# Kernel tuning notes

Hardware: AMD Instinct MI355X
Metric: run time of the kernel (lower is better)

Reference implementation:

```python
import jax, jax.numpy as jnp
import numpy as np

I, H, T, B, T2 = 512, 1024, 384, 128, 384  # input_size, hidden, cell seq, batch, gru seq


def _gru_layer(x, h0, Wih, Whh, bih, bhh):
    """PyTorch-style GRU layer. x: (B,T,Cin), h0: (B,H). Returns (out (B,T,H), h_last (B,H))."""
    xg = jnp.einsum('btc,gc->btg', x, Wih) + bih  # (B,T,3H) input projections, precomputed

    def step(h, xg_t):
        gh = h @ Whh.T + bhh                      # (B,3H)
        xr, xz, xn = jnp.split(xg_t, 3, axis=-1)
        hr, hz, hn = jnp.split(gh, 3, axis=-1)
        r = jax.nn.sigmoid(xr + hr)
        z = jax.nn.sigmoid(xz + hz)
        n = jnp.tanh(xn + r * hn)
        h_new = (1.0 - z) * n + z * h
        return h_new, h_new

    h_last, ys = jax.lax.scan(step, h0, jnp.swapaxes(xg, 0, 1))  # scan over T
    return jnp.swapaxes(ys, 0, 1), h_last


def setup_inputs() -> dict:
    key = jax.random.key(0)
    ks = jax.random.split(key, 16)
    bound = 1.0 / np.sqrt(H)
    u = lambda kk, shape: jax.random.uniform(kk, shape, jnp.float32, -bound, bound)
    return {
        'input_seq': jax.random.normal(ks[0], (T, B, I), jnp.float32),
        'rand_input': jax.random.normal(ks[1], (B, T2, H), jnp.float32),
        'h0': jax.random.normal(ks[2], (2, B, H), jnp.float32),
        'cell_Wih': u(ks[3], (3 * H, I)),
        'cell_Whh': u(ks[4], (3 * H, H)),
        'cell_bih': u(ks[5], (3 * H,)),
        'cell_bhh': u(ks[6], (3 * H,)),
        'gru_Wih0': u(ks[7], (3 * H, H)),
        'gru_Whh0': u(ks[8], (3 * H, H)),
        'gru_bih0': u(ks[9], (3 * H,)),
        'gru_bhh0': u(ks[10], (3 * H,)),
        'gru_Wih1': u(ks[11], (3 * H, H)),
        'gru_Whh1': u(ks[12], (3 * H, H)),
        'gru_bih1': u(ks[13], (3 * H,)),
        'gru_bhh1': u(ks[14], (3 * H,)),
        'lin_W': u(ks[15], (1, H)),
        'lin_b': jnp.zeros((1,), jnp.float32),
    }


def reference(input_seq, rand_input, h0,
              cell_Wih, cell_Whh, cell_bih, cell_bhh,
              gru_Wih0, gru_Whh0, gru_bih0, gru_bhh0,
              gru_Wih1, gru_Whh1, gru_bih1, gru_bhh1,
              lin_W, lin_b):
    # --- GRUCellModel: cell called with hx=None each step -> hidden is zeros every
    # step, so the whole 'recurrence' vectorizes over T (h @ Whh == 0).
    xg = jnp.einsum('tbi,gi->tbg', input_seq, cell_Wih) + cell_bih  # (T,B,3H)
    xr, xz, xn = jnp.split(xg, 3, axis=-1)
    br, bz, bn = jnp.split(cell_bhh, 3)
    r = jax.nn.sigmoid(xr + br)
    z = jax.nn.sigmoid(xz + bz)
    n = jnp.tanh(xn + r * bn)
    gru_cell_output = jnp.swapaxes((1.0 - z) * n, 0, 1)  # (B,T,H); unused downstream (as in source)

    # --- GRUModel: ignores its input, runs 2-layer GRU on internal random tensors.
    out0, _ = _gru_layer(rand_input, h0[0], gru_Wih0, gru_Whh0, gru_bih0, gru_bhh0)
    gru_output, _ = _gru_layer(out0, h0[1], gru_Wih1, gru_Whh1, gru_bih1, gru_bhh1)

    s = gru_output.shape[1] // 3
    outputs = jnp.concatenate([gru_output[:, 0:s], gru_output[:, s:2 * s], gru_output[:, 2 * s:]], axis=1)

    # second GRU run, zero initial hidden; keep last layer's final hidden
    zero_h = jnp.zeros((outputs.shape[0], H), outputs.dtype)
    o0, _ = _gru_layer(outputs, zero_h, gru_Wih0, gru_Whh0, gru_bih0, gru_bhh0)
    _, h_last = _gru_layer(o0, zero_h, gru_Wih1, gru_Whh1, gru_bih1, gru_bhh1)

    predictions = h_last @ lin_W.T + lin_b  # (B,1)
    # anchor: keep the (dead-code) GRUCell branch alive under jit without changing values
    predictions = predictions + 0.0 * jnp.sum(gru_cell_output)
    return predictions
```

## Files before the change

kernel.cpp:

```cpp
#include <hip/hip_runtime.h>
#include <math.h>

typedef __attribute__((ext_vector_type(8))) __bf16          bf16x8;
typedef __attribute__((ext_vector_type(8))) unsigned short  ushort8;
typedef __attribute__((ext_vector_type(4))) float           f32x4;
typedef __attribute__((ext_vector_type(4))) unsigned int    u32x4;

constexpr int Bb = 128, Hh = 1024, Tt = 384, BH = Bb * Hh;
constexpr int NWG = 256, BLK = 256;

constexpr size_t SLOT_B  = 524288;
constexpr size_t OFF_H   = 1024;
constexpr size_t OFF_W   = OFF_H + 8 * SLOT_B;
constexpr size_t WBLK_B  = 12288;
constexpr size_t OFF_X   = OFF_W + 4096ull * WBLK_B;
constexpr size_t WS_FULL = OFF_X + 384ull * SLOT_B;

__device__ __forceinline__ float b2f(unsigned short h) {
    unsigned u = ((unsigned)h) << 16;
    return __builtin_bit_cast(float, u);
}
__device__ __forceinline__ void split_bf16(float x, unsigned short& hi, unsigned short& lo) {
    unsigned u  = __builtin_bit_cast(unsigned, x);
    unsigned uh = u & 0xFFFF0000u;
    hi = (unsigned short)(uh >> 16);
    float rem = x - __builtin_bit_cast(float, uh);
    unsigned ur = __builtin_bit_cast(unsigned, rem);
    ur += 0x7FFFu + ((ur >> 16) & 1u);
    lo = (unsigned short)(ur >> 16);
}
__device__ __forceinline__ void split8(const float* src, ushort8& h8, ushort8& l8) {
    const float4* p4 = (const float4*)src;
    float4 a = p4[0], b = p4[1];
    float v[8] = {a.x, a.y, a.z, a.w, b.x, b.y, b.z, b.w};
    #pragma unroll
    for (int m = 0; m < 8; ++m) { unsigned short h, l; split_bf16(v[m], h, l); h8[m] = h; l8[m] = l; }
}
__device__ __forceinline__ void async16(const void* g, void* l) {
    __builtin_amdgcn_global_load_lds(
        (const __attribute__((address_space(1))) unsigned int*)g,
        (__attribute__((address_space(3))) unsigned int*)l, 16, 0, 0);
}


__global__ void wsplit_kernel(const float* __restrict__ W0i, const float* __restrict__ W0h,
                              const float* __restrict__ W1i, const float* __restrict__ W1h,
                              char* __restrict__ wbuf) {
    int t = blockIdx.x * 256 + threadIdx.x;
    if (t >= 4 * 64 * 16 * 48 * 8) return;
    int g8 = t & 7;
    int r  = (t >> 3) % 48;
    int rest = (t >> 3) / 48;
    int kcg = rest & 15, jwg = (rest >> 4) & 63, m = rest >> 10;
    const float* W = (m == 0) ? W0i : (m == 1) ? W0h : (m == 2) ? W1i : W1h;
    int ct = r >> 4, jl = r & 15;
    const float* src = W + (size_t)((ct << 10) + jwg * 16 + jl) * 1024 + kcg * 64 + g8 * 8;
    ushort8 h8, l8; split8(src, h8, l8);
    int ks = (g8 >> 2) & 1, kg = g8 & 3, lane = kg * 16 + jl;
    char* blk = wbuf + (size_t)rest * WBLK_B;
    int off0 = (ct * 4 + ks) * 1024 + lane * 16;
    *(ushort8*)(blk + off0)        = h8;
    *(ushort8*)(blk + off0 + 2048) = l8;
}

__global__ void xsplit_kernel(const float* __restrict__ xin, char* __restrict__ xb) {
    int t = blockIdx.x * 256 + threadIdx.x;
    if (t >= 384 * 128 * 128) return;
    int g8 = t & 127, b = (t >> 7) & 127, tau = t >> 14;
    const float* src = xin + ((size_t)b * 384 + tau) * 1024 + g8 * 8;
    ushort8 h8, l8; split8(src, h8, l8);
    int kcg = g8 >> 3, gin = g8 & 7;
    int ks = (gin >> 2) & 1, kg = gin & 3;
    int lane = kg * 16 + (b & 15);
    int BI0 = kcg * 32 + (b >> 5) * 8 + ((b >> 4) & 1) * 4 + ks;
    char* dst = xb + (size_t)tau * SLOT_B + (size_t)BI0 * 1024 + lane * 16;
    *(ushort8*)dst          = h8;
    *(ushort8*)(dst + 2048) = l8;
}

__global__ void hinit_kernel(const float* __restrict__ h0, char* __restrict__ ws) {
    int t = blockIdx.x * 256 + threadIdx.x;
    if (t == 0) *(unsigned*)ws = 0;
    if (t >= 4 * 128 * 128) return;
    char* hs = ws + OFF_H;
    int g8 = t & 127, b = (t >> 7) & 127, si = t >> 14;
    ushort8 h8, l8;
    if (si < 2) {
        split8(h0 + (size_t)si * BH + (size_t)b * 1024 + g8 * 8, h8, l8);
    } else {
        #pragma unroll
        for (int m = 0; m < 8; ++m) { h8[m] = 0; l8[m] = 0; }
    }
    int kcg = g8 >> 3, gin = g8 & 7;
    int ks = (gin >> 2) & 1, kg = gin & 3;
    int lane = kg * 16 + (b & 15);
    int BI0 = kcg * 32 + (b >> 5) * 8 + ((b >> 4) & 1) * 4 + ks;
    char* dst = hs + (size_t)(si * 2 + 1) * SLOT_B + (size_t)BI0 * 1024 + lane * 16;
    *(ushort8*)dst          = h8;
    *(ushort8*)(dst + 2048) = l8;
}


__device__ __forceinline__ void grid_barrier(unsigned* cnt, unsigned target) {
    __syncthreads();
    if (threadIdx.x == 0) {
        __hip_atomic_fetch_add(cnt, 1u, __ATOMIC_RELEASE, __HIP_MEMORY_SCOPE_AGENT);
        while (__hip_atomic_load(cnt, __ATOMIC_RELAXED, __HIP_MEMORY_SCOPE_AGENT) < target)
            __builtin_amdgcn_s_sleep(1);
    }
    __syncthreads();
}

#define WAITVM(N) asm volatile("s_waitcnt vmcnt(" #N ")" ::: "memory")

#define GITER(CH, SLOT, ACC, WN, DOISS)                                  \
    WAITVM(WN);                                                          \
    asm volatile("" ::: "memory");                                       \
    __builtin_amdgcn_s_barrier();                                        \
    __builtin_amdgcn_sched_barrier(0);                                   \
    if (DOISS) { issueA((CH) + 3, ar[((SLOT) + 3) & 3]);                 \
                 issueB((CH) + 3, ((SLOT) + 3) & 3); }                   \
    computeC(ar[SLOT], (SLOT), ACC);

template<bool XS>
__global__ __launch_bounds__(BLK, 2) void gru_persistent(
    const float* __restrict__ xin,
    const float* __restrict__ bih0, const float* __restrict__ bhh0,
    const float* __restrict__ bih1, const float* __restrict__ bhh1,
    unsigned* __restrict__ cnt, char* __restrict__ ws)
{
    __shared__ char Bs[4][12288];

    char*       hs = ws + OFF_H;
    const char* wb = ws + OFF_W;
    const char* xs = ws + OFF_X;

    const int bid = blockIdx.x, layer = bid >> 6, jwg = bid & 63, jbase = jwg * 16;
    const int tid = threadIdx.x, lane = tid & 63, rg = tid >> 6;

    const float* bih = (layer & 1) ? bih1 : bih0;
    const float* bhh = (layer & 1) ? bhh1 : bhh0;
    const int jl = lane & 15;
    const int jcol = jbase + jl;
    const float b_ir = bih[jcol],          b_hr = bhh[jcol];
    const float b_iz = bih[Hh + jcol],     b_hz = bhh[Hh + jcol];
    const float b_in = bih[2 * Hh + jcol], b_hn = bhh[2 * Hh + jcol];

    const int kcg_j = jcol >> 6, ks_j = (jcol >> 5) & 1, kg_j = (jcol >> 3) & 3, e_j = jcol & 7;
    const int baseBI = kcg_j * 32 + rg * 8 + ks_j;
    auto hoff = [&](int rb, int pl, int q) -> size_t {
        return (size_t)(baseBI + rb * 4 + pl * 2) * 1024
             + (size_t)(kg_j * 16 + (lane >> 4) * 4 + q) * 16 + e_j * 2;
    };

    float hreg[8];
    const bool fb0 = (!XS) && (layer == 0);

    unsigned target = NWG;
    for (int s = 0; s < Tt + 3; ++s, target += NWG) {
        const int tau = s - layer;
        if (tau >= 0 && tau < Tt) {
            const char* Axb = (layer == 0) ? (xs + (size_t)tau * SLOT_B)
                                           : (hs + (size_t)(((layer - 1) * 2) + (tau & 1)) * SLOT_B);
            const char* Ahb = hs + (size_t)((layer * 2) + ((tau - 1) & 1)) * SLOT_B;
            char*       Hd  = hs + (size_t)((layer * 2) + (tau & 1)) * SLOT_B;

            if (tau == 0) {
                if (layer < 2) {
                    #pragma unroll
                    for (int rb = 0; rb < 2; ++rb)
                        #pragma unroll
                        for (int q = 0; q < 4; ++q) {
                            unsigned short hi = __hip_atomic_load(
                                (const unsigned short*)(Ahb + hoff(rb, 0, q)),
                                __ATOMIC_RELAXED, __HIP_MEMORY_SCOPE_AGENT);
                            unsigned short lo = __hip_atomic_load(
                                (const unsigned short*)(Ahb + hoff(rb, 1, q)),
                                __ATOMIC_RELAXED, __HIP_MEMORY_SCOPE_AGENT);
                            hreg[rb * 4 + q] = b2f(hi) + b2f(lo);
                        }
                    asm volatile("s_waitcnt vmcnt(0)" ::: "memory");
                } else {
                    #pragma unroll
                    for (int i = 0; i < 8; ++i) hreg[i] = 0.f;
                }
            }

            auto issueA = [&](int ch, u32x4* fr) {
                const char* base = ((ch < 16) ? Axb : Ahb)
                                 + ((size_t)(ch & 15) << 15) + (rg << 13) + (lane << 4);
                #pragma unroll
                for (int rb = 0; rb < 2; ++rb) {
                    const char* p = base + (rb << 12);
                    asm volatile("global_load_dwordx4 %0, %1, off sc0 sc1"             : "=v"(fr[rb*4+0]) : "v"(p));
                    asm volatile("global_load_dwordx4 %0, %1, off offset:1024 sc0 sc1" : "=v"(fr[rb*4+1]) : "v"(p));
                    asm volatile("global_load_dwordx4 %0, %1, off offset:2048 sc0 sc1" : "=v"(fr[rb*4+2]) : "v"(p));
                    asm volatile("global_load_dwordx4 %0, %1, off offset:3072 sc0 sc1" : "=v"(fr[rb*4+3]) : "v"(p));
                }
            };
            auto issueB = [&](int ch, int buf) {
                const int m = (layer & 1) * 2 + (ch < 16 ? 0 : 1);
                const char* Wb = wb + (size_t)(((m * 64 + jwg) << 4) + (ch & 15)) * WBLK_B;
                char* L = &Bs[buf][0];
                #pragma unroll
                for (int i = 0; i < 3; ++i) {
                    int seg = rg + i * 4;
                    async16(Wb + seg * 1024 + lane * 16, L + seg * 1024);
                }
            };
            auto fragX = [&](int ch, u32x4* fr) {
                const int kcg = ch & 15;
                #pragma unroll
                for (int rb = 0; rb < 2; ++rb)
                    #pragma unroll
                    for (int ks = 0; ks < 2; ++ks) {
                        int row = rg * 32 + rb * 16 + (lane & 15);
                        int k0  = kcg * 64 + ks * 32 + (lane >> 4) * 8;
                        ushort8 h8, l8;
                        split8(xin + ((size_t)row * 384 + tau) * 1024 + k0, h8, l8);
                        fr[rb * 4 + ks]     = __builtin_bit_cast(u32x4, h8);
                        fr[rb * 4 + 2 + ks] = __builtin_bit_cast(u32x4, l8);
                    }
            };
            auto computeC = [&](u32x4* fr, int buf, f32x4 (&acc)[2][3]) {
                const char* B = &Bs[buf][0];
                __builtin_amdgcn_s_setprio(1);
                #pragma unroll
                for (int ks = 0; ks < 2; ++ks) {
                    bf16x8 Bh[3], Bl[3];
                    #pragma unroll
                    for (int ct = 0; ct < 3; ++ct) {
                        Bh[ct] = __builtin_bit_cast(bf16x8, *(const ushort8*)(B + (ct*4 + ks)*1024 + lane*16));
                        Bl[ct] = __builtin_bit_cast(bf16x8, *(const ushort8*)(B + (ct*4 + 2 + ks)*1024 + lane*16));
                    }
                    #pragma unroll
                    for (int rb = 0; rb < 2; ++rb) {
                        bf16x8 Ah = __builtin_bit_cast(bf16x8, fr[rb*4 + ks]);
                        bf16x8 Al = __builtin_bit_cast(bf16x8, fr[rb*4 + 2 + ks]);
                        #pragma unroll
                        for (int ct = 0; ct < 3; ++ct) {
                            f32x4 c = acc[rb][ct];
                            c = __builtin_amdgcn_mfma_f32_16x16x32_bf16(Ah, Bh[ct], c, 0, 0, 0);
                            c = __builtin_amdgcn_mfma_f32_16x16x32_bf16(Al, Bh[ct], c, 0, 0, 0);
                            c = __builtin_amdgcn_mfma_f32_16x16x32_bf16(Ah, Bl[ct], c, 0, 0, 0);
                            acc[rb][ct] = c;
                        }
                    }
                }
                __builtin_amdgcn_s_setprio(0);
            };

            f32x4 accX[2][3], accH[2][3];
            const f32x4 zv = {0.f, 0.f, 0.f, 0.f};
            #pragma unroll
            for (int rb = 0; rb < 2; ++rb)
                #pragma unroll
                for (int ct = 0; ct < 3; ++ct) { accX[rb][ct] = zv; accH[rb][ct] = zv; }

            u32x4 ar[4][8];

            if (!fb0) {
                issueA(0, ar[0]); issueB(0, 0);
                issueA(1, ar[1]); issueB(1, 1);
                issueA(2, ar[2]); issueB(2, 2);
                for (int c4 = 0; c4 < 16; c4 += 4) {
                    GITER(c4 + 0, 0, accX, 22, true);
                    GITER(c4 + 1, 1, accX, 22, true);
                    GITER(c4 + 2, 2, accX, 22, true);
                    GITER(c4 + 3, 3, accX, 22, true);
                }
                for (int c4 = 16; c4 < 28; c4 += 4) {
                    GITER(c4 + 0, 0, accH, 22, true);
                    GITER(c4 + 1, 1, accH, 22, true);
                    GITER(c4 + 2, 2, accH, 22, true);
                    GITER(c4 + 3, 3, accH, 22, true);
                }
                GITER(28, 0, accH, 22, true);
                GITER(29, 1, accH, 22, false);
                GITER(30, 2, accH, 11, false);
                GITER(31, 3, accH, 0,  false);
            } else {
                for (int ch = 0; ch < 32; ++ch) {
                    if (ch < 16) fragX(ch, ar[0]); else issueA(ch, ar[0]);
                    issueB(ch, 0);
                    asm volatile("s_waitcnt vmcnt(0)" ::: "memory");
                    asm volatile("" ::: "memory");
                    __builtin_amdgcn_s_barrier();
                    __builtin_amdgcn_sched_barrier(0);
                    if (ch < 16) computeC(ar[0], 0, accX); else computeC(ar[0], 0, accH);
                    asm volatile("" ::: "memory");
                    __builtin_amdgcn_s_barrier();
                    asm volatile("" ::: "memory");
                }
            }

            #pragma unroll
            for (int rb = 0; rb < 2; ++rb)
                #pragma unroll
                for (int q = 0; q < 4; ++q) {
                    float rp = accX[rb][0][q] + accH[rb][0][q] + b_ir + b_hr;
                    float zp = accX[rb][1][q] + accH[rb][1][q] + b_iz + b_hz;
                    float xn = accX[rb][2][q] + b_in;
                    float hn = accH[rb][2][q] + b_hn;
                    float r  = 1.0f / (1.0f + expf(-rp));
                    float z  = 1.0f / (1.0f + expf(-zp));
                    float n  = tanhf(xn + r * hn);
                    float h  = (1.0f - z) * n + z * hreg[rb * 4 + q];
                    hreg[rb * 4 + q] = h;
                    unsigned short hi, lo; split_bf16(h, hi, lo);
                    __hip_atomic_store((unsigned short*)(Hd + hoff(rb, 0, q)), hi,
                                       __ATOMIC_RELAXED, __HIP_MEMORY_SCOPE_AGENT);
                    __hip_atomic_store((unsigned short*)(Hd + hoff(rb, 1, q)), lo,
                                       __ATOMIC_RELAXED, __HIP_MEMORY_SCOPE_AGENT);
                }
        }
        grid_barrier(cnt, target);
    }
}

__global__ void pred_kernel(const char* __restrict__ hs,
                            const float* __restrict__ linW,
                            const float* __restrict__ linb,
                            float* __restrict__ out) {
    const int b = blockIdx.x, l = threadIdx.x;
    const char* slot = hs + 7 * SLOT_B;
    const int rpart = (b >> 5) * 8 + ((b >> 4) & 1) * 4;
    float s = 0.f;
    for (int u = l; u < Hh; u += 64) {
        int BI0 = (u >> 6) * 32 + rpart + ((u >> 5) & 1);
        size_t o = (size_t)BI0 * 1024 + (size_t)(((u >> 3) & 3) * 16 + (b & 15)) * 16 + (u & 7) * 2;
        float hv = b2f(*(const unsigned short*)(slot + o))
                 + b2f(*(const unsigned short*)(slot + o + 2048));
        s += hv * linW[u];
    }
    #pragma unroll
    for (int off = 32; off > 0; off >>= 1) s += __shfl_down(s, off);
    if (l == 0) out[b] = s + linb[0];
}

extern "C" void kernel_launch(void* const* d_in, const int* in_sizes, int n_in,
                              void* d_out, int out_size, void* d_ws, size_t ws_size,
                              hipStream_t stream) {
    const float* rand_in = (const float*)d_in[1];
    const float* h0      = (const float*)d_in[2];
    const float* Wih0    = (const float*)d_in[7];
    const float* Whh0    = (const float*)d_in[8];
    const float* bih0    = (const float*)d_in[9];
    const float* bhh0    = (const float*)d_in[10];
    const float* Wih1    = (const float*)d_in[11];
    const float* Whh1    = (const float*)d_in[12];
    const float* bih1    = (const float*)d_in[13];
    const float* bhh1    = (const float*)d_in[14];
    const float* linW    = (const float*)d_in[15];
    const float* linb    = (const float*)d_in[16];
    float* out = (float*)d_out;

    char*     ws  = (char*)d_ws;
    unsigned* cnt = (unsigned*)d_ws;
    char*     hsl = ws + OFF_H;

    const bool xsl = (ws_size >= WS_FULL);

    wsplit_kernel<<<6144, 256, 0, stream>>>(Wih0, Whh0, Wih1, Whh1, ws + OFF_W);
    hinit_kernel<<<256, 256, 0, stream>>>(h0, ws);
    if (xsl) {
        xsplit_kernel<<<24576, 256, 0, stream>>>(rand_in, ws + OFF_X);
        gru_persistent<true><<<NWG, BLK, 0, stream>>>(rand_in, bih0, bhh0, bih1, bhh1, cnt, ws);
    } else {
        gru_persistent<false><<<NWG, BLK, 0, stream>>>(rand_in, bih0, bhh0, bih1, bhh1, cnt, ws);
    }
    pred_kernel<<<Bb, 64, 0, stream>>>(hsl, linW, linb, out);
}
```

Baseline: 14.61 ms.

## Retile GRU persistent kernel to 32 columns by 64 rows per workgroup

```diff
diff --git a/kernel.cpp b/kernel.cpp
--- a/kernel.cpp
+++ b/kernel.cpp
@@ -12,8 +12,8 @@
 constexpr size_t SLOT_B  = 524288;
 constexpr size_t OFF_H   = 1024;
 constexpr size_t OFF_W   = OFF_H + 8 * SLOT_B;
-constexpr size_t WBLK_B  = 12288;
-constexpr size_t OFF_X   = OFF_W + 4096ull * WBLK_B;
+constexpr size_t WBLK_B  = 24576;
+constexpr size_t OFF_X   = OFF_W + 2048ull * WBLK_B;
 constexpr size_t WS_FULL = OFF_X + 384ull * SLOT_B;
 
 __device__ __forceinline__ float b2f(unsigned short h) {
@@ -47,14 +47,15 @@
                               const float* __restrict__ W1i, const float* __restrict__ W1h,
                               char* __restrict__ wbuf) {
     int t = blockIdx.x * 256 + threadIdx.x;
-    if (t >= 4 * 64 * 16 * 48 * 8) return;
+    if (t >= 2048 * 96 * 8) return;
     int g8 = t & 7;
-    int r  = (t >> 3) % 48;
-    int rest = (t >> 3) / 48;
-    int kcg = rest & 15, jwg = (rest >> 4) & 63, m = rest >> 10;
+    int r  = (t >> 3) % 96;
+    int rest = (t >> 3) / 96;
+    int kcg = rest & 15, cg = (rest >> 4) & 31, m = rest >> 9;
     const float* W = (m == 0) ? W0i : (m == 1) ? W0h : (m == 2) ? W1i : W1h;
     int ct = r >> 4, jl = r & 15;
-    const float* src = W + (size_t)((ct << 10) + jwg * 16 + jl) * 1024 + kcg * 64 + g8 * 8;
+    int jh = ct / 3, g = ct % 3;
+    const float* src = W + (size_t)((g << 10) + cg * 32 + jh * 16 + jl) * 1024 + kcg * 64 + g8 * 8;
     ushort8 h8, l8; split8(src, h8, l8);
     int ks = (g8 >> 2) & 1, kg = g8 & 3, lane = kg * 16 + jl;
     char* blk = wbuf + (size_t)rest * WBLK_B;
@@ -123,34 +124,43 @@
     computeC(ar[SLOT], (SLOT), ACC);
 
 template<bool XS>
-__global__ __launch_bounds__(BLK, 2) void gru_persistent(
+__global__ __launch_bounds__(BLK, 1) void gru_persistent(
     const float* __restrict__ xin,
     const float* __restrict__ bih0, const float* __restrict__ bhh0,
     const float* __restrict__ bih1, const float* __restrict__ bhh1,
     unsigned* __restrict__ cnt, char* __restrict__ ws)
 {
-    __shared__ char Bs[4][12288];
+    __shared__ char Bs[4][24576];
 
     char*       hs = ws + OFF_H;
     const char* wb = ws + OFF_W;
     const char* xs = ws + OFF_X;
 
-    const int bid = blockIdx.x, layer = bid >> 6, jwg = bid & 63, jbase = jwg * 16;
-    const int tid = threadIdx.x, lane = tid & 63, rg = tid >> 6;
+    const int bid = blockIdx.x;
+    const int xcd = bid & 7, sl = bid >> 3;
+    const int pair = xcd * 16 + (sl >> 1), rq = sl & 1;
+    const int layer = pair >> 5, cg = pair & 31;
+    const int tid = threadIdx.x, lane = tid & 63, wv = tid >> 6;
 
     const float* bih = (layer & 1) ? bih1 : bih0;
     const float* bhh = (layer & 1) ? bhh1 : bhh0;
     const int jl = lane & 15;
-    const int jcol = jbase + jl;
-    const float b_ir = bih[jcol],          b_hr = bhh[jcol];
-    const float b_iz = bih[Hh + jcol],     b_hz = bhh[Hh + jcol];
-    const float b_in = bih[2 * Hh + jcol], b_hn = bhh[2 * Hh + jcol];
-
-    const int kcg_j = jcol >> 6, ks_j = (jcol >> 5) & 1, kg_j = (jcol >> 3) & 3, e_j = jcol & 7;
-    const int baseBI = kcg_j * 32 + rg * 8 + ks_j;
-    auto hoff = [&](int rb, int pl, int q) -> size_t {
-        return (size_t)(baseBI + rb * 4 + pl * 2) * 1024
-             + (size_t)(kg_j * 16 + (lane >> 4) * 4 + q) * 16 + e_j * 2;
+
+    int   kcg_j[2], ks_j[2], kg_j[2], e_j[2];
+    float b_ir[2], b_hr[2], b_iz[2], b_hz[2], b_in[2], b_hn[2];
+    #pragma unroll
+    for (int jh = 0; jh < 2; ++jh) {
+        int j = cg * 32 + jh * 16 + jl;
+        kcg_j[jh] = j >> 6; ks_j[jh] = (j >> 5) & 1; kg_j[jh] = (j >> 3) & 3; e_j[jh] = j & 7;
+        b_ir[jh] = bih[j];           b_hr[jh] = bhh[j];
+        b_iz[jh] = bih[Hh + j];      b_hz[jh] = bhh[Hh + j];
+        b_in[jh] = bih[2 * Hh + j];  b_hn[jh] = bhh[2 * Hh + j];
+    }
+    const int rowBI = (rq * 2 + (wv >> 1)) * 8 + (wv & 1) * 4;
+
+    auto hoff = [&](int jh, int pl, int q) -> size_t {
+        return (size_t)(kcg_j[jh] * 32 + rowBI + pl * 2 + ks_j[jh]) * 1024
+             + (size_t)(kg_j[jh] * 16 + (lane >> 4) * 4 + q) * 16 + e_j[jh] * 2;
     };
 
     float hreg[8];
@@ -168,16 +178,16 @@
             if (tau == 0) {
                 if (layer < 2) {
                     #pragma unroll
-                    for (int rb = 0; rb < 2; ++rb)
+                    for (int jh = 0; jh < 2; ++jh)
                         #pragma unroll
                         for (int q = 0; q < 4; ++q) {
                             unsigned short hi = __hip_atomic_load(
-                                (const unsigned short*)(Ahb + hoff(rb, 0, q)),
+                                (const unsigned short*)(Ahb + hoff(jh, 0, q)),
                                 __ATOMIC_RELAXED, __HIP_MEMORY_SCOPE_AGENT);
                             unsigned short lo = __hip_atomic_load(
-                                (const unsigned short*)(Ahb + hoff(rb, 1, q)),
+                                (const unsigned short*)(Ahb + hoff(jh, 1, q)),
                                 __ATOMIC_RELAXED, __HIP_MEMORY_SCOPE_AGENT);
-                            hreg[rb * 4 + q] = b2f(hi) + b2f(lo);
+                            hreg[jh * 4 + q] = b2f(hi) + b2f(lo);
                         }
                     asm volatile("s_waitcnt vmcnt(0)" ::: "memory");
                 } else {
@@ -187,97 +197,89 @@
             }
 
             auto issueA = [&](int ch, u32x4* fr) {
-                const char* base = ((ch < 16) ? Axb : Ahb)
-                                 + ((size_t)(ch & 15) << 15) + (rg << 13) + (lane << 4);
-                #pragma unroll
-                for (int rb = 0; rb < 2; ++rb) {
-                    const char* p = base + (rb << 12);
-                    asm volatile("global_load_dwordx4 %0, %1, off sc0 sc1"             : "=v"(fr[rb*4+0]) : "v"(p));
-                    asm volatile("global_load_dwordx4 %0, %1, off offset:1024 sc0 sc1" : "=v"(fr[rb*4+1]) : "v"(p));
-                    asm volatile("global_load_dwordx4 %0, %1, off offset:2048 sc0 sc1" : "=v"(fr[rb*4+2]) : "v"(p));
-                    asm volatile("global_load_dwordx4 %0, %1, off offset:3072 sc0 sc1" : "=v"(fr[rb*4+3]) : "v"(p));
+                const char* p = ((ch < 16) ? Axb : Ahb)
+                              + ((size_t)(ch & 15) << 15) + ((size_t)rowBI << 10) + (lane << 4);
+                if (!(ch < 16 && layer == 0)) {
+                    asm volatile("global_load_dwordx4 %0, %1, off sc0 sc1"             : "=v"(fr[0]) : "v"(p));
+                    asm volatile("global_load_dwordx4 %0, %1, off offset:1024 sc0 sc1" : "=v"(fr[1]) : "v"(p));
+                    asm volatile("global_load_dwordx4 %0, %1, off offset:2048 sc0 sc1" : "=v"(fr[2]) : "v"(p));
+                    asm volatile("global_load_dwordx4 %0, %1, off offset:3072 sc0 sc1" : "=v"(fr[3]) : "v"(p));
+                } else {
+                    asm volatile("global_load_dwordx4 %0, %1, off"             : "=v"(fr[0]) : "v"(p));
+                    asm volatile("global_load_dwordx4 %0, %1, off offset:1024" : "=v"(fr[1]) : "v"(p));
+                    asm volatile("global_load_dwordx4 %0, %1, off offset:2048" : "=v"(fr[2]) : "v"(p));
+                    asm volatile("global_load_dwordx4 %0, %1, off offset:3072" : "=v"(fr[3]) : "v"(p));
                 }
             };
             auto issueB = [&](int ch, int buf) {
                 const int m = (layer & 1) * 2 + (ch < 16 ? 0 : 1);
-                const char* Wb = wb + (size_t)(((m * 64 + jwg) << 4) + (ch & 15)) * WBLK_B;
+                const char* Wb = wb + (size_t)(((m * 32 + cg) << 4) + (ch & 15)) * WBLK_B;
                 char* L = &Bs[buf][0];
                 #pragma unroll
-                for (int i = 0; i < 3; ++i) {
-                    int seg = rg + i * 4;
+                for (int i = 0; i < 6; ++i) {
+                    int seg = wv + i * 4;
                     async16(Wb + seg * 1024 + lane * 16, L + seg * 1024);
                 }
             };
             auto fragX = [&](int ch, u32x4* fr) {
                 const int kcg = ch & 15;
                 #pragma unroll
-                for (int rb = 0; rb < 2; ++rb)
-                    #pragma unroll
-                    for (int ks = 0; ks < 2; ++ks) {
-                        int row = rg * 32 + rb * 16 + (lane & 15);
-                        int k0  = kcg * 64 + ks * 32 + (lane >> 4) * 8;
-                        ushort8 h8, l8;
-                        split8(xin + ((size_t)row * 384 + tau) * 1024 + k0, h8, l8);
-                        fr[rb * 4 + ks]     = __builtin_bit_cast(u32x4, h8);
-                        fr[rb * 4 + 2 + ks] = __builtin_bit_cast(u32x4, l8);
-                    }
+                for (int ks = 0; ks < 2; ++ks) {
+                    int row = rq * 64 + wv * 16 + (lane & 15);
+                    int k0  = kcg * 64 + ks * 32 + (lane >> 4) * 8;
+                    ushort8 h8, l8;
+                    split8(xin + ((size_t)row * 384 + tau) * 1024 + k0, h8, l8);
+                    fr[ks]     = __builtin_bit_cast(u32x4, h8);
+                    fr[2 + ks] = __builtin_bit_cast(u32x4, l8);
+                }
             };
-            auto computeC = [&](u32x4* fr, int buf, f32x4 (&acc)[2][3]) {
+            auto computeC = [&](u32x4* fr, int buf, f32x4 (&acc)[6]) {
                 const char* B = &Bs[buf][0];
                 __builtin_amdgcn_s_setprio(1);
                 #pragma unroll
                 for (int ks = 0; ks < 2; ++ks) {
-                    bf16x8 Bh[3], Bl[3];
+                    bf16x8 Ah = __builtin_bit_cast(bf16x8, fr[ks]);
+                    bf16x8 Al = __builtin_bit_cast(bf16x8, fr[2 + ks]);
                     #pragma unroll
-                    for (int ct = 0; ct < 3; ++ct) {
-                        Bh[ct] = __builtin_bit_cast(bf16x8, *(const ushort8*)(B + (ct*4 + ks)*1024 + lane*16));
-                        Bl[ct] = __builtin_bit_cast(bf16x8, *(const ushort8*)(B + (ct*4 + 2 + ks)*1024 + lane*16));
-                    }
-                    #pragma unroll
-                    for (int rb = 0; rb < 2; ++rb) {
-                        bf16x8 Ah = __builtin_bit_cast(bf16x8, fr[rb*4 + ks]);
-                        bf16x8 Al = __builtin_bit_cast(bf16x8, fr[rb*4 + 2 + ks]);
-                        #pragma unroll
-                        for (int ct = 0; ct < 3; ++ct) {
-                            f32x4 c = acc[rb][ct];
-                            c = __builtin_amdgcn_mfma_f32_16x16x32_bf16(Ah, Bh[ct], c, 0, 0, 0);
-                            c = __builtin_amdgcn_mfma_f32_16x16x32_bf16(Al, Bh[ct], c, 0, 0, 0);
-                            c = __builtin_amdgcn_mfma_f32_16x16x32_bf16(Ah, Bl[ct], c, 0, 0, 0);
-                            acc[rb][ct] = c;
-                        }
+                    for (int ct = 0; ct < 6; ++ct) {
+                        bf16x8 Bh = __builtin_bit_cast(bf16x8, *(const ushort8*)(B + (ct*4 + ks)*1024 + lane*16));
+                        bf16x8 Bl = __builtin_bit_cast(bf16x8, *(const ushort8*)(B + (ct*4 + ks)*1024 + 2048 + lane*16));
+                        f32x4 c = acc[ct];
+                        c = __builtin_amdgcn_mfma_f32_16x16x32_bf16(Ah, Bh, c, 0, 0, 0);
+                        c = __builtin_amdgcn_mfma_f32_16x16x32_bf16(Al, Bh, c, 0, 0, 0);
+                        c = __builtin_amdgcn_mfma_f32_16x16x32_bf16(Ah, Bl, c, 0, 0, 0);
+                        acc[ct] = c;
                     }
                 }
                 __builtin_amdgcn_s_setprio(0);
             };
 
-            f32x4 accX[2][3], accH[2][3];
+            f32x4 accX[6], accH[6];
             const f32x4 zv = {0.f, 0.f, 0.f, 0.f};
             #pragma unroll
-            for (int rb = 0; rb < 2; ++rb)
-                #pragma unroll
-                for (int ct = 0; ct < 3; ++ct) { accX[rb][ct] = zv; accH[rb][ct] = zv; }
-
-            u32x4 ar[4][8];
+            for (int ct = 0; ct < 6; ++ct) { accX[ct] = zv; accH[ct] = zv; }
+
+            u32x4 ar[4][4];
 
             if (!fb0) {
                 issueA(0, ar[0]); issueB(0, 0);
                 issueA(1, ar[1]); issueB(1, 1);
                 issueA(2, ar[2]); issueB(2, 2);
                 for (int c4 = 0; c4 < 16; c4 += 4) {
-                    GITER(c4 + 0, 0, accX, 22, true);
-                    GITER(c4 + 1, 1, accX, 22, true);
-                    GITER(c4 + 2, 2, accX, 22, true);
-                    GITER(c4 + 3, 3, accX, 22, true);
+                    GITER(c4 + 0, 0, accX, 20, true);
+                    GITER(c4 + 1, 1, accX, 20, true);
+                    GITER(c4 + 2, 2, accX, 20, true);
+                    GITER(c4 + 3, 3, accX, 20, true);
                 }
                 for (int c4 = 16; c4 < 28; c4 += 4) {
-                    GITER(c4 + 0, 0, accH, 22, true);
-                    GITER(c4 + 1, 1, accH, 22, true);
-                    GITER(c4 + 2, 2, accH, 22, true);
-                    GITER(c4 + 3, 3, accH, 22, true);
-                }
-                GITER(28, 0, accH, 22, true);
-                GITER(29, 1, accH, 22, false);
-                GITER(30, 2, accH, 11, false);
+                    GITER(c4 + 0, 0, accH, 20, true);
+                    GITER(c4 + 1, 1, accH, 20, true);
+                    GITER(c4 + 2, 2, accH, 20, true);
+                    GITER(c4 + 3, 3, accH, 20, true);
+                }
+                GITER(28, 0, accH, 20, true);
+                GITER(29, 1, accH, 20, false);
+                GITER(30, 2, accH, 10, false);
                 GITER(31, 3, accH, 0,  false);
             } else {
                 for (int ch = 0; ch < 32; ++ch) {
@@ -295,22 +297,22 @@
             }
 
             #pragma unroll
-            for (int rb = 0; rb < 2; ++rb)
+            for (int jh = 0; jh < 2; ++jh)
                 #pragma unroll
                 for (int q = 0; q < 4; ++q) {
-                    float rp = accX[rb][0][q] + accH[rb][0][q] + b_ir + b_hr;
-                    float zp = accX[rb][1][q] + accH[rb][1][q] + b_iz + b_hz;
-                    float xn = accX[rb][2][q] + b_in;
-                    float hn = accH[rb][2][q] + b_hn;
+                    float rp = accX[jh*3 + 0][q] + accH[jh*3 + 0][q] + b_ir[jh] + b_hr[jh];
+                    float zp = accX[jh*3 + 1][q] + accH[jh*3 + 1][q] + b_iz[jh] + b_hz[jh];
+                    float xn = accX[jh*3 + 2][q] + b_in[jh];
+                    float hn = accH[jh*3 + 2][q] + b_hn[jh];
                     float r  = 1.0f / (1.0f + expf(-rp));
                     float z  = 1.0f / (1.0f + expf(-zp));
                     float n  = tanhf(xn + r * hn);
-                    float h  = (1.0f - z) * n + z * hreg[rb * 4 + q];
-                    hreg[rb * 4 + q] = h;
+                    float h  = (1.0f - z) * n + z * hreg[jh * 4 + q];
+                    hreg[jh * 4 + q] = h;
                     unsigned short hi, lo; split_bf16(h, hi, lo);
-                    __hip_atomic_store((unsigned short*)(Hd + hoff(rb, 0, q)), hi,
+                    __hip_atomic_store((unsigned short*)(Hd + hoff(jh, 0, q)), hi,
                                        __ATOMIC_RELAXED, __HIP_MEMORY_SCOPE_AGENT);
-                    __hip_atomic_store((unsigned short*)(Hd + hoff(rb, 1, q)), lo,
+                    __hip_atomic_store((unsigned short*)(Hd + hoff(jh, 1, q)), lo,
                                        __ATOMIC_RELAXED, __HIP_MEMORY_SCOPE_AGENT);
                 }
         }
```

New measurement: 14.96 ms. +2.4%, slower.

## Give every GRU timestep its own hidden-state buffer and drop coherent loads

Applied to the files above, without the earlier changes.

```diff
diff --git a/kernel.cpp b/kernel.cpp
--- a/kernel.cpp
+++ b/kernel.cpp
@@ -15,6 +15,8 @@
 constexpr size_t WBLK_B  = 12288;
 constexpr size_t OFF_X   = OFF_W + 4096ull * WBLK_B;
 constexpr size_t WS_FULL = OFF_X + 384ull * SLOT_B;
+constexpr size_t OFF_R   = WS_FULL;
+constexpr size_t WS_ROT  = OFF_R + 4ull * 385 * SLOT_B;
 
 __device__ __forceinline__ float b2f(unsigned short h) {
     unsigned u = ((unsigned)h) << 16;
@@ -78,7 +80,7 @@
     *(ushort8*)(dst + 2048) = l8;
 }
 
-__global__ void hinit_kernel(const float* __restrict__ h0, char* __restrict__ ws) {
+__global__ void hinit_kernel(const float* __restrict__ h0, char* __restrict__ ws, int rot) {
     int t = blockIdx.x * 256 + threadIdx.x;
     if (t == 0) *(unsigned*)ws = 0;
     if (t >= 4 * 128 * 128) return;
@@ -95,9 +97,15 @@
     int ks = (gin >> 2) & 1, kg = gin & 3;
     int lane = kg * 16 + (b & 15);
     int BI0 = kcg * 32 + (b >> 5) * 8 + ((b >> 4) & 1) * 4 + ks;
-    char* dst = hs + (size_t)(si * 2 + 1) * SLOT_B + (size_t)BI0 * 1024 + lane * 16;
+    size_t foff = (size_t)BI0 * 1024 + lane * 16;
+    char* dst = hs + (size_t)(si * 2 + 1) * SLOT_B + foff;
     *(ushort8*)dst          = h8;
     *(ushort8*)(dst + 2048) = l8;
+    if (rot) {
+        char* dr = ws + OFF_R + (size_t)(si * 385) * SLOT_B + foff;
+        *(ushort8*)dr          = h8;
+        *(ushort8*)(dr + 2048) = l8;
+    }
 }
 
 
@@ -122,7 +130,7 @@
                  issueB((CH) + 3, ((SLOT) + 3) & 3); }                   \
     computeC(ar[SLOT], (SLOT), ACC);
 
-template<bool XS>
+template<int MODE>
 __global__ __launch_bounds__(BLK, 2) void gru_persistent(
     const float* __restrict__ xin,
     const float* __restrict__ bih0, const float* __restrict__ bhh0,
@@ -134,6 +142,7 @@
     char*       hs = ws + OFF_H;
     const char* wb = ws + OFF_W;
     const char* xs = ws + OFF_X;
+    char*       rt = ws + OFF_R;
 
     const int bid = blockIdx.x, layer = bid >> 6, jwg = bid & 63, jbase = jwg * 16;
     const int tid = threadIdx.x, lane = tid & 63, rg = tid >> 6;
@@ -154,16 +163,24 @@
     };
 
     float hreg[8];
-    const bool fb0 = (!XS) && (layer == 0);
+    const bool fb0 = (MODE == 0) && (layer == 0);
 
     unsigned target = NWG;
     for (int s = 0; s < Tt + 3; ++s, target += NWG) {
         const int tau = s - layer;
         if (tau >= 0 && tau < Tt) {
-            const char* Axb = (layer == 0) ? (xs + (size_t)tau * SLOT_B)
-                                           : (hs + (size_t)(((layer - 1) * 2) + (tau & 1)) * SLOT_B);
-            const char* Ahb = hs + (size_t)((layer * 2) + ((tau - 1) & 1)) * SLOT_B;
-            char*       Hd  = hs + (size_t)((layer * 2) + (tau & 1)) * SLOT_B;
+            const char *Axb, *Ahb; char* Hd;
+            if (MODE == 2) {
+                Axb = (layer == 0) ? (xs + (size_t)tau * SLOT_B)
+                                   : (rt + (size_t)((layer - 1) * 385 + tau + 1) * SLOT_B);
+                Ahb = rt + (size_t)(layer * 385 + tau) * SLOT_B;
+                Hd  = rt + (size_t)(layer * 385 + tau + 1) * SLOT_B;
+            } else {
+                Axb = (layer == 0) ? (xs + (size_t)tau * SLOT_B)
+                                   : (hs + (size_t)(((layer - 1) * 2) + (tau & 1)) * SLOT_B);
+                Ahb = hs + (size_t)((layer * 2) + ((tau - 1) & 1)) * SLOT_B;
+                Hd  = hs + (size_t)((layer * 2) + (tau & 1)) * SLOT_B;
+            }
 
             if (tau == 0) {
                 if (layer < 2) {
@@ -171,12 +188,16 @@
                     for (int rb = 0; rb < 2; ++rb)
                         #pragma unroll
                         for (int q = 0; q < 4; ++q) {
-                            unsigned short hi = __hip_atomic_load(
-                                (const unsigned short*)(Ahb + hoff(rb, 0, q)),
-                                __ATOMIC_RELAXED, __HIP_MEMORY_SCOPE_AGENT);
-                            unsigned short lo = __hip_atomic_load(
-                                (const unsigned short*)(Ahb + hoff(rb, 1, q)),
-                                __ATOMIC_RELAXED, __HIP_MEMORY_SCOPE_AGENT);
+                            unsigned short hi, lo;
+                            if (MODE == 2) {
+                                hi = *(const unsigned short*)(Ahb + hoff(rb, 0, q));
+                                lo = *(const unsigned short*)(Ahb + hoff(rb, 1, q));
+                            } else {
+                                hi = __hip_atomic_load((const unsigned short*)(Ahb + hoff(rb, 0, q)),
+                                                       __ATOMIC_RELAXED, __HIP_MEMORY_SCOPE_AGENT);
+                                lo = __hip_atomic_load((const unsigned short*)(Ahb + hoff(rb, 1, q)),
+                                                       __ATOMIC_RELAXED, __HIP_MEMORY_SCOPE_AGENT);
+                            }
                             hreg[rb * 4 + q] = b2f(hi) + b2f(lo);
                         }
                     asm volatile("s_waitcnt vmcnt(0)" ::: "memory");
@@ -189,13 +210,21 @@
             auto issueA = [&](int ch, u32x4* fr) {
                 const char* base = ((ch < 16) ? Axb : Ahb)
                                  + ((size_t)(ch & 15) << 15) + (rg << 13) + (lane << 4);
+                const bool coh = (MODE != 2) && !(ch < 16 && layer == 0);
                 #pragma unroll
                 for (int rb = 0; rb < 2; ++rb) {
                     const char* p = base + (rb << 12);
-                    asm volatile("global_load_dwordx4 %0, %1, off sc0 sc1"             : "=v"(fr[rb*4+0]) : "v"(p));
-                    asm volatile("global_load_dwordx4 %0, %1, off offset:1024 sc0 sc1" : "=v"(fr[rb*4+1]) : "v"(p));
-                    asm volatile("global_load_dwordx4 %0, %1, off offset:2048 sc0 sc1" : "=v"(fr[rb*4+2]) : "v"(p));
-                    asm volatile("global_load_dwordx4 %0, %1, off offset:3072 sc0 sc1" : "=v"(fr[rb*4+3]) : "v"(p));
+                    if (coh) {
+                        asm volatile("global_load_dwordx4 %0, %1, off sc0 sc1"             : "=v"(fr[rb*4+0]) : "v"(p));
+                        asm volatile("global_load_dwordx4 %0, %1, off offset:1024 sc0 sc1" : "=v"(fr[rb*4+1]) : "v"(p));
+                        asm volatile("global_load_dwordx4 %0, %1, off offset:2048 sc0 sc1" : "=v"(fr[rb*4+2]) : "v"(p));
+                        asm volatile("global_load_dwordx4 %0, %1, off offset:3072 sc0 sc1" : "=v"(fr[rb*4+3]) : "v"(p));
+                    } else {
+                        asm volatile("global_load_dwordx4 %0, %1, off"             : "=v"(fr[rb*4+0]) : "v"(p));
+                        asm volatile("global_load_dwordx4 %0, %1, off offset:1024" : "=v"(fr[rb*4+1]) : "v"(p));
+                        asm volatile("global_load_dwordx4 %0, %1, off offset:2048" : "=v"(fr[rb*4+2]) : "v"(p));
+                        asm volatile("global_load_dwordx4 %0, %1, off offset:3072" : "=v"(fr[rb*4+3]) : "v"(p));
+                    }
                 }
             };
             auto issueB = [&](int ch, int buf) {
@@ -318,12 +347,11 @@
     }
 }
 
-__global__ void pred_kernel(const char* __restrict__ hs,
+__global__ void pred_kernel(const char* __restrict__ slot,
                             const float* __restrict__ linW,
                             const float* __restrict__ linb,
                             float* __restrict__ out) {
     const int b = blockIdx.x, l = threadIdx.x;
-    const char* slot = hs + 7 * SLOT_B;
     const int rpart = (b >> 5) * 8 + ((b >> 4) & 1) * 4;
     float s = 0.f;
     for (int u = l; u < Hh; u += 64) {
@@ -357,17 +385,24 @@
 
     char*     ws  = (char*)d_ws;
     unsigned* cnt = (unsigned*)d_ws;
-    char*     hsl = ws + OFF_H;
-
+
+    const bool rot = (ws_size >= WS_ROT);
     const bool xsl = (ws_size >= WS_FULL);
 
     wsplit_kernel<<<6144, 256, 0, stream>>>(Wih0, Whh0, Wih1, Whh1, ws + OFF_W);
-    hinit_kernel<<<256, 256, 0, stream>>>(h0, ws);
-    if (xsl) {
+    hinit_kernel<<<256, 256, 0, stream>>>(h0, ws, rot ? 1 : 0);
+    const char* pslot;
+    if (rot) {
         xsplit_kernel<<<24576, 256, 0, stream>>>(rand_in, ws + OFF_X);
-        gru_persistent<true><<<NWG, BLK, 0, stream>>>(rand_in, bih0, bhh0, bih1, bhh1, cnt, ws);
+        gru_persistent<2><<<NWG, BLK, 0, stream>>>(rand_in, bih0, bhh0, bih1, bhh1, cnt, ws);
+        pslot = ws + OFF_R + (size_t)(3 * 385 + 384) * SLOT_B;
+    } else if (xsl) {
+        xsplit_kernel<<<24576, 256, 0, stream>>>(rand_in, ws + OFF_X);
+        gru_persistent<1><<<NWG, BLK, 0, stream>>>(rand_in, bih0, bhh0, bih1, bhh1, cnt, ws);
+        pslot = ws + OFF_H + 7 * SLOT_B;
     } else {
-        gru_persistent<false><<<NWG, BLK, 0, stream>>>(rand_in, bih0, bhh0, bih1, bhh1, cnt, ws);
-    }
-    pred_kernel<<<Bb, 64, 0, stream>>>(hsl, linW, linb, out);
-}
+        gru_persistent<0><<<NWG, BLK, 0, stream>>>(rand_in, bih0, bhh0, bih1, bhh1, cnt, ws);
+        pslot = ws + OFF_H + 7 * SLOT_B;
+    }
+    pred_kernel<<<Bb, 64, 0, stream>>>(pslot, linW, linb, out);
+}
```

Measured after the change: 14.53 ms. No clear change (-0.6%).
